# Kernel tuning notes

Hardware: AMD Instinct MI355X
Metric: run time of the kernel (lower is better)

## Reference

```python
import jax, jax.numpy as jnp
import numpy as np

B, N, E = 256, 4096, 65536  # graphs, nodes/graph (64*64), edges/graph


def setup_inputs() -> dict:
    key = jax.random.key(0)
    k = jax.random.split(key, 6)
    x = jax.random.normal(k[0], (B, N, 3), dtype=jnp.float32)
    src = jax.random.randint(k[1], (E,), 0, N, dtype=jnp.int32)
    dst = jax.random.randint(k[2], (E,), 0, N, dtype=jnp.int32)
    W1 = jax.random.normal(k[3], (3, 64), dtype=jnp.float32) * 0.3
    b1 = jnp.zeros((64,), dtype=jnp.float32)
    Wfc = jax.random.normal(k[4], (N * 64, 1), dtype=jnp.float32) * 0.002
    bfc = jnp.zeros((1,), dtype=jnp.float32)
    return {"x": x, "W1": W1, "b1": b1, "Wfc": Wfc, "bfc": bfc,
            "src": src, "dst": dst}


def reference(x, W1, b1, Wfc, bfc, src, dst):
    # DGL GraphConv, norm='both': h = relu(D_in^{-1/2} A D_out^{-1/2} x W + b)
    ones = jnp.ones((E,), dtype=x.dtype)
    deg_out = jax.ops.segment_sum(ones, src, num_segments=N)
    deg_in = jax.ops.segment_sum(ones, dst, num_segments=N)
    c_src = jax.lax.rsqrt(jnp.maximum(deg_out, 1.0))  # [N]
    c_dst = jax.lax.rsqrt(jnp.maximum(deg_in, 1.0))   # [N]
    # gather normalized source features, scatter-add into destinations
    msg = (x * c_src[None, :, None])[:, src]          # [B, E, 3]
    agg = jnp.zeros_like(x).at[:, dst].add(msg)       # [B, N, 3]
    h = jax.nn.relu((agg * c_dst[None, :, None]) @ W1 + b1)  # [B, N, 64]
    # fc: flatten per graph, Linear(N*64 -> 1) + sigmoid
    logits = h.reshape(x.shape[0], -1) @ Wfc + bfc    # [B, 1]
    return jax.nn.sigmoid(logits)
```

## Files before the change

kernel.cpp:

```cpp
#include <hip/hip_runtime.h>
#include <math.h>

#define Bg 256
#define Nn 4096
#define Ee 65536
#define Kk (Nn * 3)

__device__ __forceinline__ unsigned bf16r(float v) {
    unsigned b = __float_as_uint(v);
    return (b + 0x7fffu + ((b >> 16) & 1u)) >> 16;
}

__global__ __launch_bounds__(256) void k_prep_transpose(const float* __restrict__ x,
                                                        const int* __restrict__ src,
                                                        const int* __restrict__ dst,
                                                        int* __restrict__ deg_out,
                                                        int* __restrict__ cursor,
                                                        int* __restrict__ csr,
                                                        uint2* __restrict__ xsb) {
    int id = blockIdx.x;
    int t = threadIdx.x;
    if (id < 512) {
        __shared__ float4 tile4[64][49];
        int k = id & 7;
        int g = id >> 3;
        int n0 = g * 64;
        int b0 = (k & 3) * 64;
        const float* xb = x + (size_t)b0 * Kk + (size_t)n0 * 3;
#pragma unroll
        for (int i = 0; i < 12; i++) {
            int idx = i * 256 + t;
            int bi = idx / 48, j = idx - bi * 48;
            tile4[bi][j] = ((const float4*)(xb + (size_t)bi * Kk))[j];
        }
        __syncthreads();
        const float* tile = (const float*)tile4;
        uint2* outp = xsb + ((size_t)k * Nn + n0) * 64;
#pragma unroll
        for (int i = 0; i < 16; i++) {
            int idx = i * 256 + t;
            int nn = idx >> 6, bl = idx & 63;
            float f0 = tile[bl * 196 + nn * 3 + 0];
            float f1 = tile[bl * 196 + nn * 3 + 1];
            float f2 = tile[bl * 196 + nn * 3 + 2];
            uint2 u;
            u.x = bf16r(f0) | (bf16r(f1) << 16);
            u.y = bf16r(f2);
            outp[(size_t)nn * 64 + bl] = u;
        }
    } else {
        int e = (id - 512) * 256 + t;
        int s = src[e], d = dst[e];
        atomicAdd(&deg_out[s], 1);
        int ofs = atomicAdd(&cursor[d], 1) & 63;
        csr[(d << 6) + ofs] = s;
    }
}

__global__ __launch_bounds__(256) void k_main(const uint2* __restrict__ xsb,
                                              const float* __restrict__ W1,
                                              const float* __restrict__ b1,
                                              const float* __restrict__ Wfc,
                                              const int* __restrict__ deg_out,
                                              const int* __restrict__ cursor,
                                              const int* __restrict__ csr,
                                              float* __restrict__ partial) {
    __shared__ float4 sW14[64];
    __shared__ float sWfc[4][64];
    __shared__ float red[4][64];
    int t = threadIdx.x & 63;
    int w = threadIdx.x >> 6;
    int sq = blockIdx.x & 7;
    int bq = blockIdx.x & 3;
    int g  = blockIdx.x >> 2;
    int n  = g * 4 + w;
    if (w == 0) sW14[t] = make_float4(W1[t], W1[64 + t], W1[128 + t], b1[t]);
    sWfc[w][t] = Wfc[n * 64 + t];
    __syncthreads();

    const uint2* slab = xsb + (size_t)sq * (Nn * 64);
    const int* row = csr + (n << 6);
    int degv = cursor[n];
    int deg = degv > 64 ? 64 : degv;
    float a0 = 0.f, a1 = 0.f, a2 = 0.f;
    float e0 = 0.f, e1 = 0.f, e2 = 0.f;
    int i = 0;
    for (; i + 4 <= deg; i += 4) {
        int s0 = row[i], s1 = row[i + 1], s2 = row[i + 2], s3 = row[i + 3];
        float q0 = rsqrtf(fmaxf((float)deg_out[s0], 1.f));
        float q1 = rsqrtf(fmaxf((float)deg_out[s1], 1.f));
        float q2 = rsqrtf(fmaxf((float)deg_out[s2], 1.f));
        float q3 = rsqrtf(fmaxf((float)deg_out[s3], 1.f));
        uint2 u0 = slab[(s0 << 6) + t];
        uint2 u1 = slab[(s1 << 6) + t];
        uint2 u2 = slab[(s2 << 6) + t];
        uint2 u3 = slab[(s3 << 6) + t];
        a0 = fmaf(__uint_as_float(u0.x << 16), q0, a0);
        a1 = fmaf(__uint_as_float(u0.x & 0xffff0000u), q0, a1);
        a2 = fmaf(__uint_as_float(u0.y << 16), q0, a2);
        e0 = fmaf(__uint_as_float(u1.x << 16), q1, e0);
        e1 = fmaf(__uint_as_float(u1.x & 0xffff0000u), q1, e1);
        e2 = fmaf(__uint_as_float(u1.y << 16), q1, e2);
        a0 = fmaf(__uint_as_float(u2.x << 16), q2, a0);
        a1 = fmaf(__uint_as_float(u2.x & 0xffff0000u), q2, a1);
        a2 = fmaf(__uint_as_float(u2.y << 16), q2, a2);
        e0 = fmaf(__uint_as_float(u3.x << 16), q3, e0);
        e1 = fmaf(__uint_as_float(u3.x & 0xffff0000u), q3, e1);
        e2 = fmaf(__uint_as_float(u3.y << 16), q3, e2);
    }
    for (; i < deg; i++) {
        int s = row[i];
        float q = rsqrtf(fmaxf((float)deg_out[s], 1.f));
        uint2 u = slab[(s << 6) + t];
        a0 = fmaf(__uint_as_float(u.x << 16), q, a0);
        a1 = fmaf(__uint_as_float(u.x & 0xffff0000u), q, a1);
        a2 = fmaf(__uint_as_float(u.y << 16), q, a2);
    }
    a0 += e0; a1 += e1; a2 += e2;
    float cd = rsqrtf(fmaxf((float)degv, 1.0f));
    a0 *= cd; a1 *= cd; a2 *= cd;

    float part = 0.f;
#pragma unroll 8
    for (int f = 0; f < 64; f++) {
        float4 wv = sW14[f];
        float h = fmaf(a0, wv.x, fmaf(a1, wv.y, fmaf(a2, wv.z, wv.w)));
        part = fmaf(fmaxf(h, 0.f), sWfc[w][f], part);
    }
    red[w][t] = part;
    __syncthreads();
    if (w == 0) {
        float tot = (red[0][t] + red[1][t]) + (red[2][t] + red[3][t]);
        partial[(size_t)g * 256 + bq * 64 + t] = tot;
    }
}

__global__ __launch_bounds__(256) void k_reduce_final(const float* __restrict__ partial,
                                                      float* __restrict__ out_acc,
                                                      int* __restrict__ ticket,
                                                      const float* __restrict__ bfc,
                                                      float* __restrict__ out) {
    __shared__ int lastflag;
    int t = threadIdx.x;
    int g0 = blockIdx.x * 16;
    float s = 0.f;
#pragma unroll
    for (int g = 0; g < 16; g++) s += partial[(size_t)(g0 + g) * 256 + t];
    atomicAdd(&out_acc[t], s);
    __threadfence();
    __syncthreads();
    if (t == 0) lastflag = (atomicAdd(ticket, 1) == 63);
    __syncthreads();
    if (lastflag) {
        float v = atomicAdd(&out_acc[t], 0.0f) + bfc[0];
        out[t] = 1.0f / (1.0f + expf(-v));
    }
}

extern "C" void kernel_launch(void* const* d_in, const int* in_sizes, int n_in,
                              void* d_out, int out_size, void* d_ws, size_t ws_size,
                              hipStream_t stream) {
    const float* x   = (const float*)d_in[0];
    const float* W1  = (const float*)d_in[1];
    const float* b1  = (const float*)d_in[2];
    const float* Wfc = (const float*)d_in[3];
    const float* bfc = (const float*)d_in[4];
    const int*   src = (const int*)d_in[5];
    const int*   dst = (const int*)d_in[6];
    float* out = (float*)d_out;

    char* ws = (char*)d_ws;
    uint2* xsb = (uint2*)ws;
    const size_t Z = (size_t)8 * Nn * 64 * 8;
    int*   deg_out = (int*)(ws + Z);
    int*   cursor  = (int*)(ws + Z + 16384);
    float* out_acc = (float*)(ws + Z + 32768);
    int*   ticket  = (int*)(ws + Z + 33792);
    int*   csr     = (int*)(ws + Z + 34816);
    float* partial = (float*)(ws + Z + 34816 + 1048576);

    hipMemsetAsync(ws + Z, 0, 34816, stream);
    k_prep_transpose<<<512 + Ee / 256, 256, 0, stream>>>(x, src, dst, deg_out, cursor, csr, xsb);
    k_main<<<1024 * 4, 256, 0, stream>>>(xsb, W1, b1, Wfc, deg_out, cursor, csr, partial);
    k_reduce_final<<<64, 256, 0, stream>>>(partial, out_acc, ticket, bfc, out);
}
```

Baseline: 113.4 us.

## Fuse final reduction into main kernel, precompute c_src, shuffle-broadcast edge lists

```diff
diff --git a/kernel.cpp b/kernel.cpp
--- a/kernel.cpp
+++ b/kernel.cpp
@@ -11,22 +11,22 @@
     return (b + 0x7fffu + ((b >> 16) & 1u)) >> 16;
 }
 
-__global__ __launch_bounds__(256) void k_prep_transpose(const float* __restrict__ x,
-                                                        const int* __restrict__ src,
-                                                        const int* __restrict__ dst,
-                                                        int* __restrict__ deg_out,
-                                                        int* __restrict__ cursor,
-                                                        int* __restrict__ csr,
-                                                        uint2* __restrict__ xsb) {
+__global__ __launch_bounds__(256) void k_pt(const float* __restrict__ x,
+                                            const int* __restrict__ src,
+                                            const int* __restrict__ dst,
+                                            int* __restrict__ deg_out,
+                                            int* __restrict__ cursor,
+                                            int* __restrict__ csr,
+                                            int* __restrict__ done,
+                                            float* __restrict__ c_srcf,
+                                            uint2* __restrict__ xsb) {
     int id = blockIdx.x;
     int t = threadIdx.x;
-    if (id < 512) {
+    if (id < 256) {
         __shared__ float4 tile4[64][49];
-        int k = id & 7;
-        int g = id >> 3;
-        int n0 = g * 64;
-        int b0 = (k & 3) * 64;
-        const float* xb = x + (size_t)b0 * Kk + (size_t)n0 * 3;
+        int bq = id >> 6;
+        int n0 = (id & 63) * 64;
+        const float* xb = x + (size_t)bq * 64 * Kk + (size_t)n0 * 3;
 #pragma unroll
         for (int i = 0; i < 12; i++) {
             int idx = i * 256 + t;
@@ -35,7 +35,7 @@
         }
         __syncthreads();
         const float* tile = (const float*)tile4;
-        uint2* outp = xsb + ((size_t)k * Nn + n0) * 64;
+        uint2* outp = xsb + ((size_t)bq * Nn + n0) * 64;
 #pragma unroll
         for (int i = 0; i < 16; i++) {
             int idx = i * 256 + t;
@@ -49,28 +49,42 @@
             outp[(size_t)nn * 64 + bl] = u;
         }
     } else {
-        int e = (id - 512) * 256 + t;
+        __shared__ int lastp;
+        int e = (id - 256) * 256 + t;
         int s = src[e], d = dst[e];
         atomicAdd(&deg_out[s], 1);
         int ofs = atomicAdd(&cursor[d], 1) & 63;
         csr[(d << 6) + ofs] = s;
+        __threadfence();
+        __syncthreads();
+        if (t == 0) lastp = (atomicAdd(done, 1) == 255);
+        __syncthreads();
+        if (lastp) {
+            for (int i = t; i < Nn; i += 256) {
+                int dv = atomicAdd(&deg_out[i], 0);
+                c_srcf[i] = rsqrtf(fmaxf((float)dv, 1.0f));
+            }
+        }
     }
 }
 
-__global__ __launch_bounds__(256) void k_main(const uint2* __restrict__ xsb,
+__global__ __launch_bounds__(256) void k_mega(const uint2* __restrict__ xsb,
                                               const float* __restrict__ W1,
                                               const float* __restrict__ b1,
                                               const float* __restrict__ Wfc,
-                                              const int* __restrict__ deg_out,
                                               const int* __restrict__ cursor,
                                               const int* __restrict__ csr,
-                                              float* __restrict__ partial) {
+                                              const float* __restrict__ c_srcf,
+                                              float* __restrict__ bins,
+                                              int* __restrict__ ticket,
+                                              const float* __restrict__ bfc,
+                                              float* __restrict__ out) {
     __shared__ float4 sW14[64];
     __shared__ float sWfc[4][64];
     __shared__ float red[4][64];
+    __shared__ int lastflag;
     int t = threadIdx.x & 63;
     int w = threadIdx.x >> 6;
-    int sq = blockIdx.x & 7;
     int bq = blockIdx.x & 3;
     int g  = blockIdx.x >> 2;
     int n  = g * 4 + w;
@@ -78,19 +92,19 @@
     sWfc[w][t] = Wfc[n * 64 + t];
     __syncthreads();
 
-    const uint2* slab = xsb + (size_t)sq * (Nn * 64);
-    const int* row = csr + (n << 6);
-    int degv = cursor[n];
-    int deg = degv > 64 ? 64 : degv;
+    const uint2* slab = xsb + (size_t)bq * (Nn * 64);
+    int deg = cursor[n]; if (deg > 64) deg = 64;
+    int myedge = csr[(n << 6) + t];
+    if (t >= deg) myedge = 0;
+    float myq = c_srcf[myedge];
     float a0 = 0.f, a1 = 0.f, a2 = 0.f;
-    float e0 = 0.f, e1 = 0.f, e2 = 0.f;
+    float c0 = 0.f, c1 = 0.f, c2 = 0.f;
     int i = 0;
     for (; i + 4 <= deg; i += 4) {
-        int s0 = row[i], s1 = row[i + 1], s2 = row[i + 2], s3 = row[i + 3];
-        float q0 = rsqrtf(fmaxf((float)deg_out[s0], 1.f));
-        float q1 = rsqrtf(fmaxf((float)deg_out[s1], 1.f));
-        float q2 = rsqrtf(fmaxf((float)deg_out[s2], 1.f));
-        float q3 = rsqrtf(fmaxf((float)deg_out[s3], 1.f));
+        int s0 = __shfl(myedge, i);     float q0 = __shfl(myq, i);
+        int s1 = __shfl(myedge, i + 1); float q1 = __shfl(myq, i + 1);
+        int s2 = __shfl(myedge, i + 2); float q2 = __shfl(myq, i + 2);
+        int s3 = __shfl(myedge, i + 3); float q3 = __shfl(myq, i + 3);
         uint2 u0 = slab[(s0 << 6) + t];
         uint2 u1 = slab[(s1 << 6) + t];
         uint2 u2 = slab[(s2 << 6) + t];
@@ -98,26 +112,26 @@
         a0 = fmaf(__uint_as_float(u0.x << 16), q0, a0);
         a1 = fmaf(__uint_as_float(u0.x & 0xffff0000u), q0, a1);
         a2 = fmaf(__uint_as_float(u0.y << 16), q0, a2);
-        e0 = fmaf(__uint_as_float(u1.x << 16), q1, e0);
-        e1 = fmaf(__uint_as_float(u1.x & 0xffff0000u), q1, e1);
-        e2 = fmaf(__uint_as_float(u1.y << 16), q1, e2);
+        c0 = fmaf(__uint_as_float(u1.x << 16), q1, c0);
+        c1 = fmaf(__uint_as_float(u1.x & 0xffff0000u), q1, c1);
+        c2 = fmaf(__uint_as_float(u1.y << 16), q1, c2);
         a0 = fmaf(__uint_as_float(u2.x << 16), q2, a0);
         a1 = fmaf(__uint_as_float(u2.x & 0xffff0000u), q2, a1);
         a2 = fmaf(__uint_as_float(u2.y << 16), q2, a2);
-        e0 = fmaf(__uint_as_float(u3.x << 16), q3, e0);
-        e1 = fmaf(__uint_as_float(u3.x & 0xffff0000u), q3, e1);
-        e2 = fmaf(__uint_as_float(u3.y << 16), q3, e2);
+        c0 = fmaf(__uint_as_float(u3.x << 16), q3, c0);
+        c1 = fmaf(__uint_as_float(u3.x & 0xffff0000u), q3, c1);
+        c2 = fmaf(__uint_as_float(u3.y << 16), q3, c2);
     }
     for (; i < deg; i++) {
-        int s = row[i];
-        float q = rsqrtf(fmaxf((float)deg_out[s], 1.f));
+        int s = __shfl(myedge, i);
+        float q = __shfl(myq, i);
         uint2 u = slab[(s << 6) + t];
         a0 = fmaf(__uint_as_float(u.x << 16), q, a0);
         a1 = fmaf(__uint_as_float(u.x & 0xffff0000u), q, a1);
         a2 = fmaf(__uint_as_float(u.y << 16), q, a2);
     }
-    a0 += e0; a1 += e1; a2 += e2;
-    float cd = rsqrtf(fmaxf((float)degv, 1.0f));
+    a0 += c0; a1 += c1; a2 += c2;
+    float cd = rsqrtf(fmaxf((float)deg, 1.0f));
     a0 *= cd; a1 *= cd; a2 *= cd;
 
     float part = 0.f;
@@ -131,29 +145,18 @@
     __syncthreads();
     if (w == 0) {
         float tot = (red[0][t] + red[1][t]) + (red[2][t] + red[3][t]);
-        partial[(size_t)g * 256 + bq * 64 + t] = tot;
+        atomicAdd(&bins[(g & 15) * 256 + bq * 64 + t], tot);
+        __threadfence();
+        if (t == 0) lastflag = (atomicAdd(ticket, 1) == 4095);
     }
-}
-
-__global__ __launch_bounds__(256) void k_reduce_final(const float* __restrict__ partial,
-                                                      float* __restrict__ out_acc,
-                                                      int* __restrict__ ticket,
-                                                      const float* __restrict__ bfc,
-                                                      float* __restrict__ out) {
-    __shared__ int lastflag;
-    int t = threadIdx.x;
-    int g0 = blockIdx.x * 16;
-    float s = 0.f;
-#pragma unroll
-    for (int g = 0; g < 16; g++) s += partial[(size_t)(g0 + g) * 256 + t];
-    atomicAdd(&out_acc[t], s);
-    __threadfence();
-    __syncthreads();
-    if (t == 0) lastflag = (atomicAdd(ticket, 1) == 63);
     __syncthreads();
     if (lastflag) {
-        float v = atomicAdd(&out_acc[t], 0.0f) + bfc[0];
-        out[t] = 1.0f / (1.0f + expf(-v));
+        int b = threadIdx.x;
+        float v = 0.f;
+#pragma unroll
+        for (int j = 0; j < 16; j++) v += atomicAdd(&bins[j * 256 + b], 0.0f);
+        v += bfc[0];
+        out[b] = 1.0f / (1.0f + expf(-v));
     }
 }
 
@@ -171,16 +174,17 @@
 
     char* ws = (char*)d_ws;
     uint2* xsb = (uint2*)ws;
-    const size_t Z = (size_t)8 * Nn * 64 * 8;
+    const size_t Z = (size_t)4 * Nn * 64 * 8;
     int*   deg_out = (int*)(ws + Z);
     int*   cursor  = (int*)(ws + Z + 16384);
-    float* out_acc = (float*)(ws + Z + 32768);
-    int*   ticket  = (int*)(ws + Z + 33792);
-    int*   csr     = (int*)(ws + Z + 34816);
-    float* partial = (float*)(ws + Z + 34816 + 1048576);
+    float* bins    = (float*)(ws + Z + 32768);
+    int*   done    = (int*)(ws + Z + 49152);
+    int*   ticket  = (int*)(ws + Z + 49156);
+    float* c_srcf  = (float*)(ws + Z + 49408);
+    int*   csr     = (int*)(ws + Z + 65792);
 
-    hipMemsetAsync(ws + Z, 0, 34816, stream);
-    k_prep_transpose<<<512 + Ee / 256, 256, 0, stream>>>(x, src, dst, deg_out, cursor, csr, xsb);
-    k_main<<<1024 * 4, 256, 0, stream>>>(xsb, W1, b1, Wfc, deg_out, cursor, csr, partial);
-    k_reduce_final<<<64, 256, 0, stream>>>(partial, out_acc, ticket, bfc, out);
+    hipMemsetAsync(ws + Z, 0, 49160, stream);
+    k_pt<<<512, 256, 0, stream>>>(x, src, dst, deg_out, cursor, csr, done, c_srcf, xsb);
+    k_mega<<<1024 * 4, 256, 0, stream>>>(xsb, W1, b1, Wfc, cursor, csr, c_srcf,
+                                         bins, ticket, bfc, out);
 }
```

New measurement: 211.8 us. 1.87x slower.
